# Kernel tuning notes

Hardware: AMD Instinct MI355X
Metric: run time of the kernel (lower is better)

The kernel has to match this reference:

```python
import jax, jax.numpy as jnp
import numpy as np

B, N1, N2, D, H = 2, 1024, 1024, 2048, 16
DH = D // H  # 128


def _rope_tables(S, d):
    inv = 1.0 / (10000.0 ** (np.arange(0, d, 2, dtype=np.float32) / d))
    ang = np.outer(np.arange(S, dtype=np.float32), inv)  # [S, d/2]
    cos = np.repeat(np.cos(ang), 2, axis=-1).astype(np.float32)  # [S, d] interleaved pairs
    sin = np.repeat(np.sin(ang), 2, axis=-1).astype(np.float32)
    return jnp.asarray(cos), jnp.asarray(sin)


def setup_inputs() -> dict:
    key = jax.random.key(0)
    ks = jax.random.split(key, 24)
    sc = 0.02
    cos1, sin1 = _rope_tables(N1, DH)
    cos2, sin2 = _rope_tables(N2, DH)
    inp = {
        'x_1': jax.random.normal(ks[0], (B, N1, D), dtype=jnp.float32),
        'x_2': jax.random.normal(ks[1], (B, N2, D), dtype=jnp.float32),
        'cos1': cos1, 'sin1': sin1, 'cos2': cos2, 'sin2': sin2,
    }
    names = ['wq1', 'wk1', 'wv1', 'wo1', 'wq2', 'wk2', 'wv2', 'wo2']
    for i, n in enumerate(names):
        inp[n] = jax.random.normal(ks[2 + i], (D, D), dtype=jnp.float32) * sc
        inp['b' + n[1:]] = jax.random.normal(ks[10 + i], (D,), dtype=jnp.float32) * sc
    return inp


def _apply_rope(x, cos, sin):
    # x: [B, H, S, DH]; interleaved-pair rotation (use_real_unbind_dim=-1)
    xr = x.reshape(*x.shape[:-1], -1, 2)
    x_real, x_imag = xr[..., 0], xr[..., 1]
    x_rot = jnp.stack([-x_imag, x_real], axis=-1).reshape(x.shape)
    return x * cos[None, None] + x_rot * sin[None, None]


def _split_heads(t):
    b, n, _ = t.shape
    return t.reshape(b, n, H, DH).transpose(0, 2, 1, 3)  # b h n c


def reference(x_1, x_2, cos1, sin1, cos2, sin2,
              wq1, bq1, wk1, bk1, wv1, bv1, wo1, bo1,
              wq2, bq2, wk2, bk2, wv2, bv2, wo2, bo2):
    len_1 = x_1.shape[1]
    q = jnp.concatenate([x_1 @ wq1 + bq1, x_2 @ wq2 + bq2], axis=1)
    k = jnp.concatenate([x_1 @ wk1 + bk1, x_2 @ wk2 + bk2], axis=1)
    v = jnp.concatenate([x_1 @ wv1 + bv1, x_2 @ wv2 + bv2], axis=1)
    q, k, v = _split_heads(q), _split_heads(k), _split_heads(v)
    q = q * (DH ** -0.5)
    # per-position RoPE on the concatenated stream == per-stream RoPE then concat
    cos = jnp.concatenate([cos1, cos2], axis=0)
    sin = jnp.concatenate([sin1, sin2], axis=0)
    q = _apply_rope(q, cos, sin)
    k = _apply_rope(k, cos, sin)
    # joint attention over both streams (independent/cross_only flags = False)
    scores = jnp.einsum('bhqd,bhkd->bhqk', q, k)
    attn = jax.nn.softmax(scores, axis=-1)
    o = jnp.einsum('bhqk,bhkd->bhqd', attn, v)
    o = o.transpose(0, 2, 1, 3).reshape(o.shape[0], -1, H * DH)  # b n (h c)
    o1 = o[:, :len_1] @ wo1 + bo1
    o2 = o[:, len_1:] @ wo2 + bo2
    return (o1, o2)
```

## Files before the change

kernel.cpp:

```cpp
#include <hip/hip_runtime.h>
#include <hip/hip_bf16.h>

typedef __attribute__((ext_vector_type(4))) float f32x4;
typedef __attribute__((ext_vector_type(8))) short short8;
typedef __attribute__((ext_vector_type(4))) unsigned short us4;
typedef __attribute__((ext_vector_type(2))) unsigned short us2;
typedef unsigned short u16;

__device__ __forceinline__ float bf2f(u16 u) {
  unsigned int x = ((unsigned int)u) << 16;
  float f; __builtin_memcpy(&f, &x, 4); return f;
}
__device__ __forceinline__ u16 f2bf(float f) {
  __hip_bfloat16 h = __float2bfloat16(f);
  u16 u; __builtin_memcpy(&u, &h, 2); return u;
}

#define GLL16(g, l) __builtin_amdgcn_global_load_lds( \
    (const __attribute__((address_space(1))) unsigned int*)(g), \
    (__attribute__((address_space(3))) unsigned int*)(l), 16, 0, 0)

#define MFMA16x32(a, b, c) __builtin_amdgcn_mfma_f32_16x16x32_bf16(a, b, c, 0, 0, 0)


__global__ __launch_bounds__(256) void k_convert_x(const float* __restrict__ x1,
                                                   const float* __restrict__ x2,
                                                   u16* __restrict__ xc) {
  int tid = blockIdx.x * 256 + threadIdx.x;
  int e = tid * 8;
  int m = e >> 11, d = e & 2047;
  int b = m >> 11, n = m & 2047;
  const float* src = (n < 1024) ? (x1 + ((b << 10) + n) * 2048 + d)
                                : (x2 + ((b << 10) + n - 1024) * 2048 + d);
  float4 v0 = *(const float4*)src;
  float4 v1 = *(const float4*)(src + 4);
  us4 a = {f2bf(v0.x), f2bf(v0.y), f2bf(v0.z), f2bf(v0.w)};
  us4 c = {f2bf(v1.x), f2bf(v1.y), f2bf(v1.z), f2bf(v1.w)};
  *(us4*)(xc + e) = a;
  *(us4*)(xc + e + 4) = c;
}

struct W8 { const float* w[8]; };

__global__ __launch_bounds__(256) void k_wt(W8 p, u16* __restrict__ wtbase) {
  __shared__ u16 lt[64][72];
  const float* W = p.w[blockIdx.z];
  u16* Wt = wtbase + (size_t)blockIdx.z * 4194304u;
  int k0 = blockIdx.x * 64, n0 = blockIdx.y * 64;
  int t = threadIdx.x;
#pragma unroll
  for (int i = 0; i < 4; ++i) {
    int lin = t + i * 256;
    int r = lin >> 4, c4 = (lin & 15) * 4;
    float4 v = *(const float4*)&W[(k0 + r) * 2048 + n0 + c4];
    us4 u = {f2bf(v.x), f2bf(v.y), f2bf(v.z), f2bf(v.w)};
    *(us4*)&lt[r][c4] = u;
  }
  __syncthreads();
#pragma unroll
  for (int i = 0; i < 8; ++i) {
    int lin = t + i * 256;
    int rd = lin >> 5, cs = (lin & 31) * 2;
    us2 u = {lt[cs][rd], lt[cs + 1][rd]};
    *(us2*)&Wt[(n0 + rd) * 2048 + k0 + cs] = u;
  }
}

__global__ __launch_bounds__(256) void k_vt(const u16* __restrict__ V, u16* __restrict__ Vt) {
  __shared__ u16 lt[64][72];
  int b = blockIdx.z;
  int s0 = blockIdx.x * 64, d0 = blockIdx.y * 64;
  int t = threadIdx.x;
#pragma unroll
  for (int i = 0; i < 2; ++i) {
    int lin = t + i * 256;
    int r = lin >> 3, c8 = (lin & 7) * 8;
    short8 v = *(const short8*)&V[(b * 2048 + s0 + r) * 2048 + d0 + c8];
    *(short8*)&lt[r][c8] = v;
  }
  __syncthreads();
#pragma unroll
  for (int i = 0; i < 8; ++i) {
    int lin = t + i * 256;
    int rd = lin >> 5, cs = (lin & 31) * 2;
    us2 u = {lt[cs][rd], lt[cs + 1][rd]};
    *(us2*)&Vt[(b * 2048 + d0 + rd) * 2048 + s0 + cs] = u;
  }
}

__global__ __launch_bounds__(256) void k_rope(u16* __restrict__ Qb, u16* __restrict__ Kb,
                                              const float* __restrict__ cos1,
                                              const float* __restrict__ sin1,
                                              const float* __restrict__ cos2,
                                              const float* __restrict__ sin2) {
  u16* T = blockIdx.y ? Kb : Qb;
  const float scale = blockIdx.y ? 1.f : 0.08838834764831843f;
  int tid = blockIdx.x * 256 + threadIdx.x;
  int e = tid * 8;
  int m = e >> 11;
  int n = m & 2047;
  int dh0 = e & 127;
  const float* cr; const float* sr;
  if (n < 1024) { cr = cos1 + n * 128; sr = sin1 + n * 128; }
  else          { cr = cos2 + (n - 1024) * 128; sr = sin2 + (n - 1024) * 128; }
  float4 c0 = *(const float4*)(cr + dh0), c1 = *(const float4*)(cr + dh0 + 4);
  float4 s0 = *(const float4*)(sr + dh0), s1 = *(const float4*)(sr + dh0 + 4);
  short8 xv = *(short8*)(T + e);
  float x0 = bf2f((u16)xv[0]), x1 = bf2f((u16)xv[1]), x2 = bf2f((u16)xv[2]), x3 = bf2f((u16)xv[3]);
  float x4 = bf2f((u16)xv[4]), x5 = bf2f((u16)xv[5]), x6 = bf2f((u16)xv[6]), x7 = bf2f((u16)xv[7]);
  us4 o0 = { f2bf((x0 * c0.x - x1 * s0.x) * scale), f2bf((x1 * c0.x + x0 * s0.x) * scale),
             f2bf((x2 * c0.z - x3 * s0.z) * scale), f2bf((x3 * c0.z + x2 * s0.z) * scale) };
  us4 o1 = { f2bf((x4 * c1.x - x5 * s1.x) * scale), f2bf((x5 * c1.x + x4 * s1.x) * scale),
             f2bf((x6 * c1.z - x7 * s1.z) * scale), f2bf((x7 * c1.z + x6 * s1.z) * scale) };
  *(us4*)(T + e) = o0;
  *(us4*)(T + e + 4) = o1;
}


__device__ __forceinline__ void gemm_core(const u16* __restrict__ A,
                                          const u16* __restrict__ Bt,
                                          u16* lA, u16* lB,
                                          f32x4 acc[4][4], int m0, int n0) {
  const int t = threadIdx.x;
  const int lane = t & 63;
  const int lq = lane & 15, lg = lane >> 4;
  const int wr = (t >> 7) & 1, wc = (t >> 6) & 1;
  for (int k0 = 0; k0 < 2048; k0 += 64) {
    __syncthreads();
#pragma unroll
    for (int i = 0; i < 4; ++i) {
      int chunk = i * 256 + t;
      int r = chunk >> 3, c = chunk & 7;
      GLL16(A + ((m0 + r) * 2048 + k0 + c * 8), lA + chunk * 8);
      GLL16(Bt + ((n0 + r) * 2048 + k0 + c * 8), lB + chunk * 8);
    }
    asm volatile("s_waitcnt vmcnt(0)" ::: "memory");
    __syncthreads();
#pragma unroll
    for (int kc = 0; kc < 2; ++kc) {
      short8 af[4], bf[4];
#pragma unroll
      for (int rf = 0; rf < 4; ++rf)
        af[rf] = *(const short8*)(lA + (wr * 64 + rf * 16 + lq) * 64 + kc * 32 + lg * 8);
#pragma unroll
      for (int cf = 0; cf < 4; ++cf)
        bf[cf] = *(const short8*)(lB + (wc * 64 + cf * 16 + lq) * 64 + kc * 32 + lg * 8);
#pragma unroll
      for (int rf = 0; rf < 4; ++rf)
#pragma unroll
        for (int cf = 0; cf < 4; ++cf)
          acc[rf][cf] = MFMA16x32(af[rf], bf[cf], acc[rf][cf]);
    }
  }
}

struct QKVP {
  const u16* wt[6];
  const float* bias[6];
  u16* out[3];
  const u16* xc;
};

__global__ __launch_bounds__(256) void k_gemm_qkv(QKVP p) {
  __shared__ u16 lA[128 * 64];
  __shared__ u16 lB[128 * 64];
  const int m0 = blockIdx.x * 128, n0 = blockIdx.y * 128;
  const int idx = blockIdx.z * 2 + ((m0 >> 10) & 1);
  f32x4 acc[4][4];
  const f32x4 z4 = {0.f, 0.f, 0.f, 0.f};
#pragma unroll
  for (int a = 0; a < 4; ++a)
#pragma unroll
    for (int b = 0; b < 4; ++b) acc[a][b] = z4;
  gemm_core(p.xc, p.wt[idx], lA, lB, acc, m0, n0);
  const float* bias = p.bias[idx];
  u16* out = p.out[blockIdx.z];
  const int lane = threadIdx.x & 63, lq = lane & 15, lg = lane >> 4;
  const int wr = (threadIdx.x >> 7) & 1, wc = (threadIdx.x >> 6) & 1;
#pragma unroll
  for (int cf = 0; cf < 4; ++cf) {
    int col = n0 + wc * 64 + cf * 16 + lq;
    float bv = bias[col];
#pragma unroll
    for (int rf = 0; rf < 4; ++rf) {
      int row0 = m0 + wr * 64 + rf * 16 + lg * 4;
#pragma unroll
      for (int j = 0; j < 4; ++j)
        out[(row0 + j) * 2048 + col] = f2bf(acc[rf][cf][j] + bv);
    }
  }
}

__global__ __launch_bounds__(256) void k_gemm_out(const u16* __restrict__ O,
                                                  const u16* __restrict__ wt0,
                                                  const u16* __restrict__ wt1,
                                                  const float* __restrict__ b0,
                                                  const float* __restrict__ b1,
                                                  float* __restrict__ out) {
  __shared__ u16 lA[128 * 64];
  __shared__ u16 lB[128 * 64];
  const int m0 = blockIdx.x * 128, n0 = blockIdx.y * 128;
  const int stream1 = (m0 >> 10) & 1;
  f32x4 acc[4][4];
  const f32x4 z4 = {0.f, 0.f, 0.f, 0.f};
#pragma unroll
  for (int a = 0; a < 4; ++a)
#pragma unroll
    for (int b = 0; b < 4; ++b) acc[a][b] = z4;
  gemm_core(O, stream1 ? wt1 : wt0, lA, lB, acc, m0, n0);
  const float* bias = stream1 ? b1 : b0;
  const int lane = threadIdx.x & 63, lq = lane & 15, lg = lane >> 4;
  const int wr = (threadIdx.x >> 7) & 1, wc = (threadIdx.x >> 6) & 1;
#pragma unroll
  for (int cf = 0; cf < 4; ++cf) {
    int col = n0 + wc * 64 + cf * 16 + lq;
    float bv = bias[col];
#pragma unroll
    for (int rf = 0; rf < 4; ++rf) {
      int row0 = m0 + wr * 64 + rf * 16 + lg * 4;
#pragma unroll
      for (int j = 0; j < 4; ++j) {
        int row = row0 + j;
        int b = row >> 11, n = row & 2047;
        float* dst = stream1 ? out + 4194304 + (((b << 10) + n - 1024) * 2048 + col)
                             : out + (((b << 10) + n) * 2048 + col);
        *dst = acc[rf][cf][j] + bv;
      }
    }
  }
}

__global__ __launch_bounds__(256) void k_attn(const u16* __restrict__ Q,
                                              const u16* __restrict__ K,
                                              const u16* __restrict__ Vt,
                                              u16* __restrict__ O) {
  __shared__ __align__(16) u16 kbuf[2][64 * 128];
  __shared__ __align__(16) u16 vbuf[2][128 * 64];
  __shared__ __align__(16) u16 pbuf[4][16 * 88];
  const int t = threadIdx.x, lane = t & 63, w = t >> 6;
  const int lq = lane & 15, g = lane >> 4;
  const int id = blockIdx.x;
  const int lgid = (id & 7) * 64 + (id >> 3);
  const int bh = lgid >> 4, qt = lgid & 15;
  const int b = bh >> 4, h = bh & 15;

  short8 qf[2][4];
#pragma unroll
  for (int u = 0; u < 2; ++u) {
    const u16* Qp = Q + (size_t)(b * 2048 + qt * 128 + w * 32 + u * 16 + lq) * 2048
                    + h * 128 + g * 8;
#pragma unroll
    for (int c = 0; c < 4; ++c) qf[u][c] = *(const short8*)(Qp + c * 32);
  }

  f32x4 oacc[2][8];
  const f32x4 z4 = {0.f, 0.f, 0.f, 0.f};
#pragma unroll
  for (int u = 0; u < 2; ++u)
#pragma unroll
    for (int dc = 0; dc < 8; ++dc) oacc[u][dc] = z4;
  float m_run[2] = {-1e30f, -1e30f}, l_run[2] = {0.f, 0.f};

  const int swz = (lq & 7) << 4;

  auto STAGE = [&](int bs, int kt) {
#pragma unroll
    for (int ii = 0; ii < 4; ++ii) {
      int i = w * 4 + ii;
      int o = i * 1024 + lane * 16;
      {
        int row = o >> 8, colb = o & 255;
        int sc = colb ^ ((row & 7) << 4);
        GLL16(K + (size_t)(b * 2048 + kt + row) * 2048 + h * 128 + (sc >> 1),
              (u16*)((char*)kbuf[bs] + o));
      }
      {
        int row = o >> 7, colb = o & 127;
        int sc = colb ^ ((row & 7) << 4);
        GLL16(Vt + (size_t)(b * 2048 + h * 128 + row) * 2048 + kt + (sc >> 1),
              (u16*)((char*)vbuf[bs] + o));
      }
    }
  };

  STAGE(0, 0);
  asm volatile("s_waitcnt vmcnt(0)" ::: "memory");
  __syncthreads();

  for (int tt = 0; tt < 32; ++tt) {
    const int cb = tt & 1;
    if (tt < 31) STAGE(cb ^ 1, (tt + 1) * 64);

    const char* kb = (const char*)kbuf[cb];
    const char* vb = (const char*)vbuf[cb];
    f32x4 s[2][4];
#pragma unroll
    for (int u = 0; u < 2; ++u)
#pragma unroll
      for (int kg = 0; kg < 4; ++kg) s[u][kg] = z4;
#pragma unroll
    for (int c = 0; c < 4; ++c) {
#pragma unroll
      for (int kg = 0; kg < 4; ++kg) {
        short8 kf = *(const short8*)(kb + (kg * 16 + lq) * 256 + ((c * 64 + g * 16) ^ swz));
        s[0][kg] = MFMA16x32(kf, qf[0][c], s[0][kg]);
        s[1][kg] = MFMA16x32(kf, qf[1][c], s[1][kg]);
      }
    }
    u16* pw = pbuf[w];
    short8 pb[2][2];
#pragma unroll
    for (int u = 0; u < 2; ++u) {
      float pm = -1e30f;
#pragma unroll
      for (int kg = 0; kg < 4; ++kg)
#pragma unroll
        for (int j = 0; j < 4; ++j) pm = fmaxf(pm, s[u][kg][j]);
      pm = fmaxf(pm, __shfl_xor(pm, 16));
      pm = fmaxf(pm, __shfl_xor(pm, 32));
      const float mnew = fmaxf(m_run[u], pm);
      const float r = __expf(m_run[u] - mnew);
      m_run[u] = mnew;
      float ps = 0.f;
#pragma unroll
      for (int kg = 0; kg < 4; ++kg) {
        float p0 = __expf(s[u][kg][0] - mnew), p1 = __expf(s[u][kg][1] - mnew);
        float p2 = __expf(s[u][kg][2] - mnew), p3 = __expf(s[u][kg][3] - mnew);
        ps += (p0 + p1) + (p2 + p3);
        us4 wv = {f2bf(p0), f2bf(p1), f2bf(p2), f2bf(p3)};
        *(us4*)(pw + lq * 88 + kg * 16 + g * 4) = wv;
      }
      ps += __shfl_xor(ps, 16);
      ps += __shfl_xor(ps, 32);
      l_run[u] = l_run[u] * r + ps;
#pragma unroll
      for (int dc = 0; dc < 8; ++dc) oacc[u][dc] = oacc[u][dc] * r;
      pb[u][0] = *(const short8*)(pw + lq * 88 + g * 8);
      pb[u][1] = *(const short8*)(pw + lq * 88 + 32 + g * 8);
    }
#pragma unroll
    for (int kc = 0; kc < 2; ++kc) {
#pragma unroll
      for (int dc = 0; dc < 8; ++dc) {
        short8 vf = *(const short8*)(vb + (dc * 16 + lq) * 128 + ((kc * 64 + g * 16) ^ swz));
        oacc[0][dc] = MFMA16x32(vf, pb[0][kc], oacc[0][dc]);
        oacc[1][dc] = MFMA16x32(vf, pb[1][kc], oacc[1][dc]);
      }
    }
    asm volatile("s_waitcnt vmcnt(0)" ::: "memory");
    __syncthreads();
  }

#pragma unroll
  for (int u = 0; u < 2; ++u) {
    const float inv = 1.f / l_run[u];
    u16* Op = O + (size_t)(b * 2048 + qt * 128 + w * 32 + u * 16 + lq) * 2048
              + h * 128 + g * 4;
#pragma unroll
    for (int dc = 0; dc < 8; ++dc) {
      us4 ov = {f2bf(oacc[u][dc][0] * inv), f2bf(oacc[u][dc][1] * inv),
                f2bf(oacc[u][dc][2] * inv), f2bf(oacc[u][dc][3] * inv)};
      *(us4*)(Op + dc * 16) = ov;
    }
  }
}


extern "C" void kernel_launch(void* const* d_in, const int* in_sizes, int n_in,
                              void* d_out, int out_size, void* d_ws, size_t ws_size,
                              hipStream_t stream) {
  const float* x1   = (const float*)d_in[0];
  const float* x2   = (const float*)d_in[1];
  const float* cos1 = (const float*)d_in[2];
  const float* sin1 = (const float*)d_in[3];
  const float* cos2 = (const float*)d_in[4];
  const float* sin2 = (const float*)d_in[5];
  W8 wp; const float* bias[8];
  for (int i = 0; i < 8; ++i) {
    wp.w[i] = (const float*)d_in[6 + 2 * i];
    bias[i] = (const float*)d_in[7 + 2 * i];
  }
  float* out = (float*)d_out;
  u16* ws = (u16*)d_ws;
  const size_t NX = 8388608;
  const size_t WSZ = 4194304;
  u16* xc = ws;
  u16* wt = ws + NX;
  u16* Qb = wt + 8 * WSZ;
  u16* Kb = Qb + NX;
  u16* Vb = Kb + NX;
  u16* Ob = Vb + NX;
  u16* Vt = xc;
  if (ws_size < (size_t)((Ob + NX) - ws) * sizeof(u16)) return;

  k_convert_x<<<dim3(4096), dim3(256), 0, stream>>>(x1, x2, xc);
  k_wt<<<dim3(32, 32, 8), dim3(256), 0, stream>>>(wp, wt);

  QKVP qp;
  qp.wt[0] = wt + 0 * WSZ; qp.wt[1] = wt + 4 * WSZ;
  qp.wt[2] = wt + 1 * WSZ; qp.wt[3] = wt + 5 * WSZ;
  qp.wt[4] = wt + 2 * WSZ; qp.wt[5] = wt + 6 * WSZ;
  qp.bias[0] = bias[0]; qp.bias[1] = bias[4];
  qp.bias[2] = bias[1]; qp.bias[3] = bias[5];
  qp.bias[4] = bias[2]; qp.bias[5] = bias[6];
  qp.out[0] = Qb; qp.out[1] = Kb; qp.out[2] = Vb;
  qp.xc = xc;
  k_gemm_qkv<<<dim3(32, 16, 3), dim3(256), 0, stream>>>(qp);

  k_rope<<<dim3(4096, 2), dim3(256), 0, stream>>>(Qb, Kb, cos1, sin1, cos2, sin2);
  k_vt<<<dim3(32, 32, 2), dim3(256), 0, stream>>>(Vb, Vt);
  k_attn<<<dim3(512), dim3(256), 0, stream>>>(Qb, Kb, Vt, Ob);
  k_gemm_out<<<dim3(32, 16), dim3(256), 0, stream>>>(Ob, wt + 3 * WSZ, wt + 7 * WSZ,
                                                     bias[3], bias[7], out);
}
```

Baseline: 391.6 us.

## Rewrite projection GEMMs with 256x128 tiles, double-buffered swizzled LDS and XCD mapping

```diff
diff --git a/kernel.cpp b/kernel.cpp
--- a/kernel.cpp
+++ b/kernel.cpp
@@ -116,115 +116,190 @@
   *(us4*)(T + e + 4) = o1;
 }
 
-
-__device__ __forceinline__ void gemm_core(const u16* __restrict__ A,
-                                          const u16* __restrict__ Bt,
-                                          u16* lA, u16* lB,
-                                          f32x4 acc[4][4], int m0, int n0) {
+__device__ __forceinline__ void gemm8_core(const u16* __restrict__ A,
+                                           const u16* __restrict__ Bt,
+                                           int m0, int nb,
+                                           u16* lA, u16* lB,
+                                           f32x4 acc[8][2]) {
   const int t = threadIdx.x;
-  const int lane = t & 63;
+  const int lane = t & 63, wid = t >> 6;
   const int lq = lane & 15, lg = lane >> 4;
-  const int wr = (t >> 7) & 1, wc = (t >> 6) & 1;
-  for (int k0 = 0; k0 < 2048; k0 += 64) {
-    __syncthreads();
-#pragma unroll
-    for (int i = 0; i < 4; ++i) {
-      int chunk = i * 256 + t;
-      int r = chunk >> 3, c = chunk & 7;
-      GLL16(A + ((m0 + r) * 2048 + k0 + c * 8), lA + chunk * 8);
-      GLL16(Bt + ((n0 + r) * 2048 + k0 + c * 8), lB + chunk * 8);
-    }
-    asm volatile("s_waitcnt vmcnt(0)" ::: "memory");
-    __syncthreads();
+  const int wr = wid >> 2, wc = wid & 3;
+  const int swz = (lq & 7) << 4;
+
+  u16* lA0 = lA;             u16* lA1 = lA + 256 * 64;
+  u16* lB0 = lB;             u16* lB1 = lB + 128 * 64;
+
+  short8 af[4][2], bf[2][2];
+
+  auto stA = [&](u16* lbase, int kt, int half) {
+    const int k0 = (kt & 31) * 64;
+#pragma unroll
+    for (int j = 0; j < 2; ++j) {
+      int r = j * 128 + half * 64 + (t >> 3);
+      int colb = (t & 7) * 16;
+      int sc = colb ^ ((r & 7) << 4);
+      GLL16(A + (size_t)(m0 + r) * 2048 + k0 + (sc >> 1),
+            (u16*)((char*)lbase + r * 128 + colb));
+    }
+  };
+  auto stB = [&](u16* lbase, int kt, int qn) {
+    const int k0 = (kt & 31) * 64;
+    int row = (t >> 7) * 32 + qn * 16 + ((t >> 3) & 15);
+    int colb = (t & 7) * 16;
+    int sc = colb ^ ((row & 7) << 4);
+    GLL16(Bt + (size_t)(nb + row) * 2048 + k0 + (sc >> 1),
+          (u16*)((char*)lbase + row * 128 + colb));
+  };
+  auto rdA = [&](const u16* lbase, int qm) {
+#pragma unroll
+    for (int mf = 0; mf < 4; ++mf)
+#pragma unroll
+      for (int kc = 0; kc < 2; ++kc) {
+        int row = wr * 128 + (qm * 4 + mf) * 16 + lq;
+        af[mf][kc] = *(const short8*)((const char*)lbase + row * 128 +
+                                      ((kc * 64 + lg * 16) ^ swz));
+      }
+  };
+  auto rdB = [&](const u16* lbase, int qn) {
 #pragma unroll
     for (int kc = 0; kc < 2; ++kc) {
-      short8 af[4], bf[4];
-#pragma unroll
-      for (int rf = 0; rf < 4; ++rf)
-        af[rf] = *(const short8*)(lA + (wr * 64 + rf * 16 + lq) * 64 + kc * 32 + lg * 8);
-#pragma unroll
-      for (int cf = 0; cf < 4; ++cf)
-        bf[cf] = *(const short8*)(lB + (wc * 64 + cf * 16 + lq) * 64 + kc * 32 + lg * 8);
-#pragma unroll
-      for (int rf = 0; rf < 4; ++rf)
-#pragma unroll
-        for (int cf = 0; cf < 4; ++cf)
-          acc[rf][cf] = MFMA16x32(af[rf], bf[cf], acc[rf][cf]);
-    }
-  }
-}
-
-struct QKVP {
+      int row = wc * 32 + qn * 16 + lq;
+      bf[qn][kc] = *(const short8*)((const char*)lbase + row * 128 +
+                                    ((kc * 64 + lg * 16) ^ swz));
+    }
+  };
+  auto mm = [&](int qm, int qn) {
+    __builtin_amdgcn_s_setprio(1);
+#pragma unroll
+    for (int mf = 0; mf < 4; ++mf)
+#pragma unroll
+      for (int kc = 0; kc < 2; ++kc)
+        acc[qm * 4 + mf][qn] = MFMA16x32(af[mf][kc], bf[qn][kc], acc[qm * 4 + mf][qn]);
+    __builtin_amdgcn_s_setprio(0);
+    __builtin_amdgcn_sched_barrier(0);
+  };
+
+#define LGK0() do { asm volatile("s_waitcnt lgkmcnt(0)" ::: "memory"); \
+                    __builtin_amdgcn_sched_barrier(0); } while (0)
+#define BAR()  __builtin_amdgcn_s_barrier()
+#define VM3()  asm volatile("s_waitcnt vmcnt(3)" ::: "memory")
+
+  stA(lA0, 0, 0); stB(lB0, 0, 0); stA(lA0, 0, 1); stB(lB0, 0, 1);
+  stA(lA1, 1, 0); stB(lB1, 1, 0);
+  VM3();
+  BAR();
+
+#pragma unroll 1
+  for (int i = 0; i < 16; ++i) {
+    const int t1 = 2 * i + 1;
+    rdA(lA0, 0); rdB(lB0, 0);
+    stA(lA1, t1, 1);
+    BAR(); LGK0(); mm(0, 0); BAR();
+    rdB(lB0, 1);
+    stB(lB1, t1, 1);
+    BAR(); LGK0(); mm(0, 1); BAR();
+    rdA(lA0, 1);
+    stA(lA0, t1 + 1, 0);
+    BAR(); LGK0(); mm(1, 0); BAR();
+    stB(lB0, t1 + 1, 0);
+    BAR(); LGK0(); mm(1, 1);
+    VM3(); BAR();
+    rdA(lA1, 0); rdB(lB1, 0);
+    stA(lA0, t1 + 1, 1);
+    BAR(); LGK0(); mm(0, 0); BAR();
+    rdB(lB1, 1);
+    stB(lB0, t1 + 1, 1);
+    BAR(); LGK0(); mm(0, 1); BAR();
+    rdA(lA1, 1);
+    stA(lA1, t1 + 2, 0);
+    BAR(); LGK0(); mm(1, 0); BAR();
+    stB(lB1, t1 + 2, 0);
+    BAR(); LGK0(); mm(1, 1);
+    VM3(); BAR();
+  }
+#undef LGK0
+#undef BAR
+#undef VM3
+}
+
+struct QKV8P {
   const u16* wt[6];
   const float* bias[6];
   u16* out[3];
   const u16* xc;
 };
 
-__global__ __launch_bounds__(256) void k_gemm_qkv(QKVP p) {
-  __shared__ u16 lA[128 * 64];
-  __shared__ u16 lB[128 * 64];
-  const int m0 = blockIdx.x * 128, n0 = blockIdx.y * 128;
-  const int idx = blockIdx.z * 2 + ((m0 >> 10) & 1);
-  f32x4 acc[4][4];
+__global__ __launch_bounds__(512, 2) void k_gemm_qkv(QKV8P p) {
+  __shared__ __align__(16) u16 lA[2 * 256 * 64];
+  __shared__ __align__(16) u16 lB[2 * 128 * 64];
+  const int id = blockIdx.x;
+  const int xcd = id & 7, wg = id >> 3;
+  const int mt = wg & 15, nt = xcd * 6 + (wg >> 4);
+  const int m0 = mt * 256;
+  const int type = nt >> 4;
+  const int colw = (nt & 15) * 128;
+  const int strm = (mt >> 2) & 1;
+  const int widx = type * 2 + strm;
+  f32x4 acc[8][2];
   const f32x4 z4 = {0.f, 0.f, 0.f, 0.f};
 #pragma unroll
-  for (int a = 0; a < 4; ++a)
-#pragma unroll
-    for (int b = 0; b < 4; ++b) acc[a][b] = z4;
-  gemm_core(p.xc, p.wt[idx], lA, lB, acc, m0, n0);
-  const float* bias = p.bias[idx];
-  u16* out = p.out[blockIdx.z];
-  const int lane = threadIdx.x & 63, lq = lane & 15, lg = lane >> 4;
-  const int wr = (threadIdx.x >> 7) & 1, wc = (threadIdx.x >> 6) & 1;
-#pragma unroll
-  for (int cf = 0; cf < 4; ++cf) {
-    int col = n0 + wc * 64 + cf * 16 + lq;
+  for (int a = 0; a < 8; ++a) { acc[a][0] = z4; acc[a][1] = z4; }
+  gemm8_core(p.xc, p.wt[widx], m0, colw, lA, lB, acc);
+  const int lane = threadIdx.x & 63, wid = threadIdx.x >> 6;
+  const int lq = lane & 15, lg = lane >> 4;
+  const int wr = wid >> 2, wc = wid & 3;
+  u16* out = p.out[type];
+  const float* bias = p.bias[widx];
+#pragma unroll
+  for (int nf = 0; nf < 2; ++nf) {
+    int col = colw + wc * 32 + nf * 16 + lq;
     float bv = bias[col];
 #pragma unroll
-    for (int rf = 0; rf < 4; ++rf) {
-      int row0 = m0 + wr * 64 + rf * 16 + lg * 4;
+    for (int mf = 0; mf < 8; ++mf) {
+      int row0 = m0 + wr * 128 + mf * 16 + lg * 4;
 #pragma unroll
       for (int j = 0; j < 4; ++j)
-        out[(row0 + j) * 2048 + col] = f2bf(acc[rf][cf][j] + bv);
-    }
-  }
-}
-
-__global__ __launch_bounds__(256) void k_gemm_out(const u16* __restrict__ O,
-                                                  const u16* __restrict__ wt0,
-                                                  const u16* __restrict__ wt1,
-                                                  const float* __restrict__ b0,
-                                                  const float* __restrict__ b1,
-                                                  float* __restrict__ out) {
-  __shared__ u16 lA[128 * 64];
-  __shared__ u16 lB[128 * 64];
-  const int m0 = blockIdx.x * 128, n0 = blockIdx.y * 128;
-  const int stream1 = (m0 >> 10) & 1;
-  f32x4 acc[4][4];
+        out[(size_t)(row0 + j) * 2048 + col] = f2bf(acc[mf][nf][j] + bv);
+    }
+  }
+}
+
+__global__ __launch_bounds__(512, 2) void k_gemm_out(const u16* __restrict__ O,
+                                                     const u16* __restrict__ wt0,
+                                                     const u16* __restrict__ wt1,
+                                                     const float* __restrict__ b0,
+                                                     const float* __restrict__ b1,
+                                                     float* __restrict__ out) {
+  __shared__ __align__(16) u16 lA[2 * 256 * 64];
+  __shared__ __align__(16) u16 lB[2 * 128 * 64];
+  const int id = blockIdx.x;
+  const int xcd = id & 7, wg = id >> 3;
+  const int mt = wg & 15, nt = xcd * 2 + (wg >> 4);
+  const int m0 = mt * 256;
+  const int strm = (mt >> 2) & 1;
+  f32x4 acc[8][2];
   const f32x4 z4 = {0.f, 0.f, 0.f, 0.f};
 #pragma unroll
-  for (int a = 0; a < 4; ++a)
-#pragma unroll
-    for (int b = 0; b < 4; ++b) acc[a][b] = z4;
-  gemm_core(O, stream1 ? wt1 : wt0, lA, lB, acc, m0, n0);
-  const float* bias = stream1 ? b1 : b0;
-  const int lane = threadIdx.x & 63, lq = lane & 15, lg = lane >> 4;
-  const int wr = (threadIdx.x >> 7) & 1, wc = (threadIdx.x >> 6) & 1;
-#pragma unroll
-  for (int cf = 0; cf < 4; ++cf) {
-    int col = n0 + wc * 64 + cf * 16 + lq;
+  for (int a = 0; a < 8; ++a) { acc[a][0] = z4; acc[a][1] = z4; }
+  gemm8_core(O, strm ? wt1 : wt0, m0, nt * 128, lA, lB, acc);
+  const float* bias = strm ? b1 : b0;
+  float* obase = strm ? out + 4194304 : out;
+  const int lane = threadIdx.x & 63, wid = threadIdx.x >> 6;
+  const int lq = lane & 15, lg = lane >> 4;
+  const int wr = wid >> 2, wc = wid & 3;
+#pragma unroll
+  for (int nf = 0; nf < 2; ++nf) {
+    int col = nt * 128 + wc * 32 + nf * 16 + lq;
     float bv = bias[col];
 #pragma unroll
-    for (int rf = 0; rf < 4; ++rf) {
-      int row0 = m0 + wr * 64 + rf * 16 + lg * 4;
+    for (int mf = 0; mf < 8; ++mf) {
+      int row0 = m0 + wr * 128 + mf * 16 + lg * 4;
 #pragma unroll
       for (int j = 0; j < 4; ++j) {
         int row = row0 + j;
         int b = row >> 11, n = row & 2047;
-        float* dst = stream1 ? out + 4194304 + (((b << 10) + n - 1024) * 2048 + col)
-                             : out + (((b << 10) + n) * 2048 + col);
-        *dst = acc[rf][cf][j] + bv;
+        obase[(size_t)(b * 1024 + n - strm * 1024) * 2048 + col] = acc[mf][nf][j] + bv;
       }
     }
   }
@@ -396,7 +471,7 @@
   k_convert_x<<<dim3(4096), dim3(256), 0, stream>>>(x1, x2, xc);
   k_wt<<<dim3(32, 32, 8), dim3(256), 0, stream>>>(wp, wt);
 
-  QKVP qp;
+  QKV8P qp;
   qp.wt[0] = wt + 0 * WSZ; qp.wt[1] = wt + 4 * WSZ;
   qp.wt[2] = wt + 1 * WSZ; qp.wt[3] = wt + 5 * WSZ;
   qp.wt[4] = wt + 2 * WSZ; qp.wt[5] = wt + 6 * WSZ;
@@ -405,11 +480,11 @@
   qp.bias[4] = bias[2]; qp.bias[5] = bias[6];
   qp.out[0] = Qb; qp.out[1] = Kb; qp.out[2] = Vb;
   qp.xc = xc;
-  k_gemm_qkv<<<dim3(32, 16, 3), dim3(256), 0, stream>>>(qp);
+  k_gemm_qkv<<<dim3(768), dim3(512), 0, stream>>>(qp);
 
   k_rope<<<dim3(4096, 2), dim3(256), 0, stream>>>(Qb, Kb, cos1, sin1, cos2, sin2);
   k_vt<<<dim3(32, 32, 2), dim3(256), 0, stream>>>(Vb, Vt);
   k_attn<<<dim3(512), dim3(256), 0, stream>>>(Qb, Kb, Vt, Ob);
-  k_gemm_out<<<dim3(32, 16), dim3(256), 0, stream>>>(Ob, wt + 3 * WSZ, wt + 7 * WSZ,
-                                                     bias[3], bias[7], out);
-}
+  k_gemm_out<<<dim3(256), dim3(512), 0, stream>>>(Ob, wt + 3 * WSZ, wt + 7 * WSZ,
+                                                  bias[3], bias[7], out);
+}
```

After: 403.0 us. +2.9%, slower.
